# Kernel optimization log

Hardware: AMD Instinct MI355X
Metric: run time of the kernel (lower is better)

Reference implementation:

```python
import jax, jax.numpy as jnp
import numpy as np

# Model dims (match init_kwargs)
B, L, D = 1, 2048, 1024
DI = 2048          # D_inner
N = 16             # SSM state size
DR = 64            # delta_rank
K = 4              # conv_1d_size
EPS = 1e-5
DELTA_MIN, DELTA_MAX, DELTA_FLOOR = 1e-3, 1e-1, 1e-4


def setup_inputs() -> dict:
    key = jax.random.key(0)
    ks = jax.random.split(key, 9)
    g = lambda i, shape, scale: (jax.random.normal(ks[i], shape, jnp.float32) * scale)
    x = g(0, (B, L, D), 1.0)
    rms_w = jnp.ones((D,), jnp.float32)
    in_proj_w = g(1, (D, 2 * DI), D ** -0.5)           # Linear D -> 2*DI, no bias
    conv_w = g(2, (DI, K), 0.3)                         # depthwise conv kernel
    conv_b = g(3, (DI,), 0.1)
    bcd_w = g(4, (DI, 2 * N + DR), DI ** -0.5)          # to_BCdelta, no bias
    dup_w = g(5, (DR, DI), DR ** -0.5)                  # delta_upscale weight
    # delta_upscale bias: inverse-softplus of log-uniform samples in [delta_min, delta_max]
    u = jax.random.uniform(ks[6], (DI,), jnp.float32)
    samples = jnp.clip(jnp.exp(u * (np.log(DELTA_MAX) - np.log(DELTA_MIN)) + np.log(DELTA_MIN)), DELTA_FLOOR)
    dup_b = samples + jnp.log(-jnp.expm1(-samples))
    # log(-A) with A = -[1..N] repeated over channels (S4D-real init)
    log_minus_A = jnp.tile(jnp.log(jnp.arange(1, N + 1, dtype=jnp.float32))[None, :], (DI, 1))
    D_param = jnp.ones((DI,), jnp.float32)              # skip parameter D
    out_proj_w = g(7, (DI, D), DI ** -0.5)              # Linear DI -> D, no bias
    return {"x": x, "rms_w": rms_w, "in_proj_w": in_proj_w, "conv_w": conv_w,
            "conv_b": conv_b, "bcd_w": bcd_w, "dup_w": dup_w, "dup_b": dup_b,
            "log_minus_A": log_minus_A, "D_param": D_param, "out_proj_w": out_proj_w}


def reference(x, rms_w, in_proj_w, conv_w, conv_b, bcd_w, dup_w, dup_b,
              log_minus_A, D_param, out_proj_w):
    b, l, _ = x.shape
    # RMSNorm
    xn = x * jax.lax.rsqrt(jnp.mean(x * x, axis=-1, keepdims=True) + EPS) * rms_w
    # in_proj and split into ssm branch / gating residual branch
    proj = xn @ in_proj_w                                  # (b,l,2*DI)
    xs, res = proj[..., :DI], proj[..., DI:]
    # causal depthwise conv1d (torch pads K-1 both sides then truncates -> left-pad only)
    xp = jnp.pad(xs, ((0, 0), (K - 1, 0), (0, 0)))         # (b,l+K-1,DI)
    conv = sum(xp[:, k:k + l, :] * conv_w[:, k] for k in range(K)) + conv_b
    xc = jax.nn.silu(conv)                                 # (b,l,DI)
    # S6 block
    bcd = xc @ bcd_w                                       # (b,l,DR+2N)
    delta_lr = bcd[..., :DR]
    Bm = bcd[..., DR:DR + N]                               # (b,l,N)
    Cm = bcd[..., DR + N:]                                 # (b,l,N)
    delta = jax.nn.softplus(delta_lr @ dup_w + dup_b)      # (b,l,DI)
    A = -jnp.exp(log_minus_A)                              # (DI,N)
    A_bar = jnp.exp(jnp.einsum('bld,dn->bldn', delta, A))  # (b,l,DI,N)
    B_bar_x = jnp.einsum('bld,bln,bld->bldn', delta, Bm, xc)
    # sequential selective scan: h_t = A_bar_t * h_{t-1} + B_bar_x_t
    def step(h, ab_bx):
        ab, bx = ab_bx
        h = ab * h + bx
        return h, h
    h0 = jnp.zeros((b, DI, N), x.dtype)
    _, hs = jax.lax.scan(step, h0, (jnp.swapaxes(A_bar, 0, 1), jnp.swapaxes(B_bar_x, 0, 1)))
    # hs: (l,b,DI,N); project out with C and add skip D
    y = jnp.einsum('bln,lbdn->bld', Cm, hs) + xc * D_param
    # gate, out_proj, residual
    y = y * jax.nn.silu(res)
    return y @ out_proj_w + x
```

## Files before the change

### kernel.cpp

```cpp
#include <hip/hip_runtime.h>
#include <hip/hip_bf16.h>
#include <math.h>

#define Lseq 2048
#define Dmod 1024
#define DI   2048
#define Nst  16
#define DRr  64
#define NCHUNK 32
#define LCHUNK 64
#define SPLITK 16

typedef unsigned short u16;
typedef float  f32x4  __attribute__((ext_vector_type(4)));
typedef short  short8 __attribute__((ext_vector_type(8)));

__device__ __forceinline__ float sigmoidf_(float x) { return 1.f / (1.f + expf(-x)); }
__device__ __forceinline__ float softplusf_(float x) {
    return fmaxf(x, 0.f) + log1pf(expf(-fabsf(x)));
}
__device__ __forceinline__ u16 f2bf(float x) {
    union { float f; unsigned u; } v; v.f = x;
    unsigned r = (v.u + 0x7fffu + ((v.u >> 16) & 1u)) >> 16;
    return (u16)r;
}
__device__ __forceinline__ float bf2f(u16 h) {
    union { unsigned u; float f; } v; v.u = ((unsigned)h) << 16; return v.f;
}
__device__ __forceinline__ void async16(const void* g, void* l) {
    __builtin_amdgcn_global_load_lds((__attribute__((address_space(1))) void*)g,
                                     (__attribute__((address_space(3))) void*)l, 16, 0, 0);
}

struct __align__(8) u16x4 { u16 x, y, z, w; };

__global__ __launch_bounds__(256) void rmsnorm_split_k(const float* __restrict__ x,
                                                       const float* __restrict__ w,
                                                       u16* __restrict__ xh,
                                                       u16* __restrict__ xl) {
    int row = blockIdx.x;
    int tid = threadIdx.x;
    float4 v = reinterpret_cast<const float4*>(x + (size_t)row * Dmod)[tid];
    float ss = v.x * v.x + v.y * v.y + v.z * v.z + v.w * v.w;
    #pragma unroll
    for (int m = 32; m >= 1; m >>= 1) ss += __shfl_xor(ss, m);
    __shared__ float s4[4];
    if ((tid & 63) == 0) s4[tid >> 6] = ss;
    __syncthreads();
    float tot = s4[0] + s4[1] + s4[2] + s4[3];
    float scale = rsqrtf(tot * (1.0f / Dmod) + 1e-5f);
    float4 wv = reinterpret_cast<const float4*>(w)[tid];
    float o[4] = {v.x * scale * wv.x, v.y * scale * wv.y,
                  v.z * scale * wv.z, v.w * scale * wv.w};
    u16x4 H, L;
    u16* hp = &H.x; u16* lp = &L.x;
    #pragma unroll
    for (int q = 0; q < 4; q++) {
        u16 h = f2bf(o[q]); hp[q] = h; lp[q] = f2bf(o[q] - bf2f(h));
    }
    reinterpret_cast<u16x4*>(xh + (size_t)row * Dmod)[tid] = H;
    reinterpret_cast<u16x4*>(xl + (size_t)row * Dmod)[tid] = L;
}

__global__ __launch_bounds__(256) void wsplitT_k(const float* __restrict__ W, int R, int Cn,
                                                 u16* __restrict__ Th, u16* __restrict__ Tl) {
    __shared__ float t[32][33];
    int r0 = blockIdx.y * 32, c0 = blockIdx.x * 32;
    int tr = threadIdx.x >> 3;
    int tc4 = (threadIdx.x & 7) * 4;
    float4 v = *reinterpret_cast<const float4*>(&W[(size_t)(r0 + tr) * Cn + c0 + tc4]);
    t[tr][tc4 + 0] = v.x; t[tr][tc4 + 1] = v.y;
    t[tr][tc4 + 2] = v.z; t[tr][tc4 + 3] = v.w;
    __syncthreads();
    u16x4 H, L;
    u16* hp = &H.x; u16* lp = &L.x;
    #pragma unroll
    for (int q = 0; q < 4; q++) {
        float xv = t[tc4 + q][tr];
        u16 h = f2bf(xv); hp[q] = h; lp[q] = f2bf(xv - bf2f(h));
    }
    size_t o = (size_t)(c0 + tr) * R + r0 + tc4;
    *reinterpret_cast<u16x4*>(&Th[o]) = H;
    *reinterpret_cast<u16x4*>(&Tl[o]) = L;
}

template <int BM, int BN, int EPI>
__global__ __launch_bounds__(256) void gemm_mfma3(
    const u16* __restrict__ Ah, const u16* __restrict__ Al,
    const u16* __restrict__ Bh, const u16* __restrict__ Bl,
    float* __restrict__ C, float* __restrict__ C2, const float* __restrict__ aux,
    int M, int N, int K) {
    constexpr int BK = 32;
    constexpr int MF = BM / 32, NF = BN / 32;
    constexpr int CH_A = BM / 16, CH_B = BN / 16;
    __shared__ u16 AhT[BM][BK], AlT[BM][BK], BhT[BN][BK], BlT[BN][BK];
    const int tid = threadIdx.x, lane = tid & 63, wid = tid >> 6;
    const int wr = wid >> 1, wc = wid & 1;
    const int lr = lane & 15, lk = (lane >> 4) * 8;
    const int bm0 = blockIdx.y * BM, bn0 = blockIdx.x * BN;
    const int srow = lane >> 2, scol = (lane & 3) * 8;

    int kbeg = 0, kend = K;
    if (EPI == 5) {
        int ks = K / gridDim.z;
        kbeg = blockIdx.z * ks;
        kend = kbeg + ks;
    }

    f32x4 acc[MF][NF];
    #pragma unroll
    for (int i = 0; i < MF; i++)
        #pragma unroll
        for (int j = 0; j < NF; j++) acc[i][j] = (f32x4){0.f, 0.f, 0.f, 0.f};

    for (int k0 = kbeg; k0 < kend; k0 += BK) {
        int ci = 0;
        #pragma unroll
        for (int c = 0; c < CH_A; c++, ci++) if ((ci & 3) == wid) {
            size_t g = (size_t)(bm0 + c * 16 + srow) * K + (k0 + scol);
            async16(Ah + g, (u16*)&AhT[0][0] + c * 512 + lane * 8);
        }
        #pragma unroll
        for (int c = 0; c < CH_A; c++, ci++) if ((ci & 3) == wid) {
            size_t g = (size_t)(bm0 + c * 16 + srow) * K + (k0 + scol);
            async16(Al + g, (u16*)&AlT[0][0] + c * 512 + lane * 8);
        }
        #pragma unroll
        for (int c = 0; c < CH_B; c++, ci++) if ((ci & 3) == wid) {
            size_t g = (size_t)(bn0 + c * 16 + srow) * K + (k0 + scol);
            async16(Bh + g, (u16*)&BhT[0][0] + c * 512 + lane * 8);
        }
        #pragma unroll
        for (int c = 0; c < CH_B; c++, ci++) if ((ci & 3) == wid) {
            size_t g = (size_t)(bn0 + c * 16 + srow) * K + (k0 + scol);
            async16(Bl + g, (u16*)&BlT[0][0] + c * 512 + lane * 8);
        }
        __syncthreads();

        short8 ah[MF], al[MF], bh[NF], bl[NF];
        #pragma unroll
        for (int i = 0; i < MF; i++) {
            int r = wr * (MF * 16) + i * 16 + lr;
            ah[i] = *(const short8*)&AhT[r][lk];
            al[i] = *(const short8*)&AlT[r][lk];
        }
        #pragma unroll
        for (int j = 0; j < NF; j++) {
            int r = wc * (NF * 16) + j * 16 + lr;
            bh[j] = *(const short8*)&BhT[r][lk];
            bl[j] = *(const short8*)&BlT[r][lk];
        }
        #pragma unroll
        for (int i = 0; i < MF; i++)
            #pragma unroll
            for (int j = 0; j < NF; j++) {
                acc[i][j] = __builtin_amdgcn_mfma_f32_16x16x32_bf16(ah[i], bh[j], acc[i][j], 0, 0, 0);
                acc[i][j] = __builtin_amdgcn_mfma_f32_16x16x32_bf16(ah[i], bl[j], acc[i][j], 0, 0, 0);
                acc[i][j] = __builtin_amdgcn_mfma_f32_16x16x32_bf16(al[i], bh[j], acc[i][j], 0, 0, 0);
            }
        __syncthreads();
    }

    float* Cp = C;
    if (EPI == 5) Cp = C + (size_t)blockIdx.z * M * N;
    #pragma unroll
    for (int i = 0; i < MF; i++)
        #pragma unroll
        for (int j = 0; j < NF; j++) {
            int rowg = bm0 + wr * (MF * 16) + i * 16 + (lane >> 4) * 4;
            int colg = bn0 + wc * (NF * 16) + j * 16 + lr;
            #pragma unroll
            for (int q = 0; q < 4; q++) {
                float v = acc[i][j][q];
                if (EPI == 0 || EPI == 5) {
                    Cp[(size_t)(rowg + q) * N + colg] = v;
                } else if (EPI == 1) {
                    size_t idx = (size_t)(rowg + q) * N + colg;
                    C[idx] = v + aux[idx];
                } else if (EPI == 2) {
                    C[(size_t)(rowg + q) * N + colg] = softplusf_(v + aux[colg]);
                } else if (EPI == 4) {
                    if (colg < DI) C[(size_t)(rowg + q) * DI + colg] = v;
                    else C2[(size_t)(rowg + q) * DI + (colg - DI)] = v * sigmoidf_(v);
                }
            }
        }
}

__global__ __launch_bounds__(256) void bcd_reduce_k(const float* __restrict__ partial,
                                                    float* __restrict__ bcd,
                                                    u16* __restrict__ bH,
                                                    u16* __restrict__ bL) {
    const int NT = Lseq * 96;
    int t = blockIdx.x * 256 + threadIdx.x;
    float s = 0.f;
    #pragma unroll
    for (int z = 0; z < SPLITK; z++) s += partial[(size_t)z * NT + t];
    bcd[t] = s;
    int col = t % 96, row = t / 96;
    if (col < DRr) {
        u16 h = f2bf(s);
        bH[(size_t)row * DRr + col] = h;
        bL[(size_t)row * DRr + col] = f2bf(s - bf2f(h));
    }
}

__global__ __launch_bounds__(256) void conv_silu_k(const float* __restrict__ xs,
                                                   const float* __restrict__ cw,
                                                   const float* __restrict__ cb,
                                                   u16* __restrict__ xcH,
                                                   u16* __restrict__ xcL) {
    int d = blockIdx.x * 256 + threadIdx.x;
    int l = blockIdx.y;
    float4 w = reinterpret_cast<const float4*>(cw)[d];
    float wk[4] = {w.x, w.y, w.z, w.w};
    float s = cb[d];
    #pragma unroll
    for (int k = 0; k < 4; k++) {
        int ls = l - 3 + k;
        if (ls >= 0) s = fmaf(xs[(size_t)ls * DI + d], wk[k], s);
    }
    float v = s * sigmoidf_(s);
    size_t o = (size_t)l * DI + d;
    u16 h = f2bf(v);
    xcH[o] = h;
    xcL[o] = f2bf(v - bf2f(h));
}

__global__ __launch_bounds__(256) void scan1_k(const float* __restrict__ delta,
                                               const u16* __restrict__ xcH,
                                               const u16* __restrict__ xcL,
                                               const float* __restrict__ bcd,
                                               const float* __restrict__ lmA,
                                               float* __restrict__ Pb,
                                               float* __restrict__ Sb) {
    __shared__ float Bs[LCHUNK][16];
    const int tid = threadIdx.x;
    const int d = (blockIdx.x * 256 + tid) >> 1;
    const int half = tid & 1;
    const int c = blockIdx.y;
    const int l0 = c * LCHUNK;
    {
        int row = tid >> 2, q = (tid & 3) * 4;
        float4 v = *reinterpret_cast<const float4*>(&bcd[(size_t)(l0 + row) * 96 + DRr + q]);
        *reinterpret_cast<float4*>(&Bs[row][q]) = v;
    }
    __syncthreads();
    float negA[8], h[8];
    #pragma unroll
    for (int j = 0; j < 8; j++) {
        negA[j] = -__expf(lmA[(size_t)d * Nst + half * 8 + j]);
        h[j] = 0.f;
    }
    float sdv = 0.f;
    for (int l = 0; l < LCHUNK; ++l) {
        size_t o = (size_t)(l0 + l) * DI + d;
        float dv = delta[o];
        float xcv = bf2f(xcH[o]) + bf2f(xcL[o]);
        sdv += dv;
        float dvx = dv * xcv;
        #pragma unroll
        for (int j = 0; j < 8; j++) {
            float a = __expf(dv * negA[j]);
            h[j] = fmaf(a, h[j], dvx * Bs[l][half * 8 + j]);
        }
    }
    size_t base = ((size_t)c * DI + d) * Nst + half * 8;
    #pragma unroll
    for (int j = 0; j < 8; j++) {
        Pb[base + j] = __expf(sdv * negA[j]);
        Sb[base + j] = h[j];
    }
}

__global__ __launch_bounds__(256) void scan2_k(float* __restrict__ PH,
                                               const float* __restrict__ Sb) {
    int t = blockIdx.x * 256 + threadIdx.x;
    float H = 0.f;
    for (int c = 0; c < NCHUNK; c++) {
        size_t idx = (size_t)c * (DI * Nst) + t;
        float P = PH[idx], S = Sb[idx];
        PH[idx] = H;
        H = S + P * H;
    }
}

__global__ __launch_bounds__(256) void scan3_k(const float* __restrict__ delta,
                                               const u16* __restrict__ xcH,
                                               const u16* __restrict__ xcL,
                                               const float* __restrict__ bcd,
                                               const float* __restrict__ lmA,
                                               const float* __restrict__ Dp,
                                               const float* __restrict__ gate,
                                               const float* __restrict__ Hinit,
                                               u16* __restrict__ yH,
                                               u16* __restrict__ yL) {
    __shared__ float BCs[LCHUNK][32];
    const int tid = threadIdx.x;
    const int d = (blockIdx.x * 256 + tid) >> 1;
    const int half = tid & 1;
    const int c = blockIdx.y;
    const int l0 = c * LCHUNK;
    #pragma unroll
    for (int i = 0; i < 2; i++) {
        int idx = tid + 256 * i;
        int row = idx >> 3, q = (idx & 7) * 4;
        float4 v = *reinterpret_cast<const float4*>(&bcd[(size_t)(l0 + row) * 96 + DRr + q]);
        *reinterpret_cast<float4*>(&BCs[row][q]) = v;
    }
    __syncthreads();
    float negA[8], h[8];
    size_t hbase = ((size_t)c * DI + d) * Nst + half * 8;
    #pragma unroll
    for (int j = 0; j < 8; j++) {
        negA[j] = -__expf(lmA[(size_t)d * Nst + half * 8 + j]);
        h[j] = Hinit[hbase + j];
    }
    float Dpv = Dp[d];
    for (int l = 0; l < LCHUNK; ++l) {
        size_t o = (size_t)(l0 + l) * DI + d;
        float dv = delta[o];
        float xcv = bf2f(xcH[o]) + bf2f(xcL[o]);
        float dvx = dv * xcv;
        float yp = 0.f;
        #pragma unroll
        for (int j = 0; j < 8; j++) {
            float a = __expf(dv * negA[j]);
            h[j] = fmaf(a, h[j], dvx * BCs[l][half * 8 + j]);
            yp = fmaf(BCs[l][16 + half * 8 + j], h[j], yp);
        }
        yp += __shfl_xor(yp, 1);
        if (half == 0) {
            float yv = (yp + xcv * Dpv) * gate[o];
            u16 hq = f2bf(yv);
            yH[o] = hq;
            yL[o] = f2bf(yv - bf2f(hq));
        }
    }
}

extern "C" void kernel_launch(void* const* d_in, const int* in_sizes, int n_in,
                              void* d_out, int out_size, void* d_ws, size_t ws_size,
                              hipStream_t stream) {
    const float* x          = (const float*)d_in[0];
    const float* rms_w      = (const float*)d_in[1];
    const float* in_proj_w  = (const float*)d_in[2];
    const float* conv_w     = (const float*)d_in[3];
    const float* conv_b     = (const float*)d_in[4];
    const float* bcd_w      = (const float*)d_in[5];
    const float* dup_w      = (const float*)d_in[6];
    const float* dup_b      = (const float*)d_in[7];
    const float* lmA        = (const float*)d_in[8];
    const float* Dp         = (const float*)d_in[9];
    const float* out_proj_w = (const float*)d_in[10];
    float* out = (float*)d_out;
    char*  W   = (char*)d_ws;

    const size_t MB = 1ull << 20;
    u16*   WiH  = (u16*)(W + 0);
    u16*   WiL  = (u16*)(W + 8 * MB);
    float* delta= (float*)(W + 0);
    float* xs   = (float*)(W + 16 * MB);
    float* part = (float*)(W + 16 * MB);
    u16*   bwTH = (u16*)(W + 28 * MB);
    u16*   bwTL = (u16*)(W + 28 * MB + 384 * 1024);
    u16*   dwTH = (u16*)(W + 28 * MB + 768 * 1024);
    u16*   dwTL = (u16*)(W + 28 * MB + 1024 * 1024);
    u16*   bcdH = (u16*)(W + 28 * MB + 1280 * 1024);
    u16*   bcdL = (u16*)(W + 28 * MB + 1536 * 1024);
    float* Sb   = (float*)(W + 16 * MB);
    u16*   yH   = (u16*)(W + 16 * MB);
    u16*   yL   = (u16*)(W + 24 * MB);
    float* gate = (float*)(W + 32 * MB);
    u16*   xcH  = (u16*)(W + 48 * MB);
    u16*   xcL  = (u16*)(W + 56 * MB);
    u16*   xnH  = (u16*)(W + 64 * MB);
    u16*   xnL  = (u16*)(W + 68 * MB);
    u16*   WoH  = (u16*)(W + 64 * MB);
    u16*   WoL  = (u16*)(W + 68 * MB);
    float* bcd  = (float*)(W + 72 * MB);
    float* Pb   = (float*)(W + 73 * MB);

    rmsnorm_split_k<<<Lseq, 256, 0, stream>>>(x, rms_w, xnH, xnL);
    wsplitT_k<<<dim3(4096 / 32, 1024 / 32), 256, 0, stream>>>(in_proj_w, 1024, 4096, WiH, WiL);
    gemm_mfma3<128, 128, 4><<<dim3(4096 / 128, Lseq / 128), 256, 0, stream>>>(
        xnH, xnL, WiH, WiL, xs, gate, nullptr, Lseq, 2 * DI, Dmod);
    conv_silu_k<<<dim3(DI / 256, Lseq), 256, 0, stream>>>(xs, conv_w, conv_b, xcH, xcL);
    wsplitT_k<<<dim3(1024 / 32, 2048 / 32), 256, 0, stream>>>(out_proj_w, 2048, 1024, WoH, WoL);
    wsplitT_k<<<dim3(96 / 32, 2048 / 32), 256, 0, stream>>>(bcd_w, 2048, 96, bwTH, bwTL);
    wsplitT_k<<<dim3(2048 / 32, 64 / 32), 256, 0, stream>>>(dup_w, 64, 2048, dwTH, dwTL);
    gemm_mfma3<128, 96, 5><<<dim3(1, Lseq / 128, SPLITK), 256, 0, stream>>>(
        xcH, xcL, bwTH, bwTL, part, nullptr, nullptr, Lseq, 96, DI);
    bcd_reduce_k<<<Lseq * 96 / 256, 256, 0, stream>>>(part, bcd, bcdH, bcdL);
    gemm_mfma3<128, 128, 2><<<dim3(DI / 128, Lseq / 128), 256, 0, stream>>>(
        bcdH, bcdL, dwTH, dwTL, delta, nullptr, dup_b, Lseq, DI, DRr);
    scan1_k<<<dim3(16, NCHUNK), 256, 0, stream>>>(delta, xcH, xcL, bcd, lmA, Pb, Sb);
    scan2_k<<<dim3(DI * Nst / 256), 256, 0, stream>>>(Pb, Sb);
    scan3_k<<<dim3(16, NCHUNK), 256, 0, stream>>>(delta, xcH, xcL, bcd, lmA, Dp, gate, Pb, yH, yL);
    gemm_mfma3<64, 128, 1><<<dim3(Dmod / 128, Lseq / 64), 256, 0, stream>>>(
        yH, yL, WoH, WoL, out, nullptr, x, Lseq, Dmod, DI);
}
```

Measured before the change: 292.1 us.

## Split-K out_proj with residual reduce, merge weight-split launches, retile in_proj

The out_proj GEMM becomes a 2-way split-K into partial buffers, and a new reduce kernel sums the partials and adds the residual x. The three small weight split/transpose kernels are merged into one launch. The in_proj GEMM switches to 128x64 tiles, which gives more blocks for better CU occupancy. The trade-off is extra partial-sum memory traffic and one more kernel launch, in exchange for more parallelism across the device.

```diff
diff --git a/kernel.cpp b/kernel.cpp
--- a/kernel.cpp
+++ b/kernel.cpp
@@ -62,10 +62,10 @@
     reinterpret_cast<u16x4*>(xl + (size_t)row * Dmod)[tid] = L;
 }
 
-__global__ __launch_bounds__(256) void wsplitT_k(const float* __restrict__ W, int R, int Cn,
-                                                 u16* __restrict__ Th, u16* __restrict__ Tl) {
-    __shared__ float t[32][33];
-    int r0 = blockIdx.y * 32, c0 = blockIdx.x * 32;
+__device__ __forceinline__ void wsplit_body(const float* __restrict__ W, int R, int Cn,
+                                            int bx, int by, float (*t)[33],
+                                            u16* __restrict__ Th, u16* __restrict__ Tl) {
+    int r0 = by * 32, c0 = bx * 32;
     int tr = threadIdx.x >> 3;
     int tc4 = (threadIdx.x & 7) * 4;
     float4 v = *reinterpret_cast<const float4*>(&W[(size_t)(r0 + tr) * Cn + c0 + tc4]);
@@ -82,6 +82,31 @@
     size_t o = (size_t)(c0 + tr) * R + r0 + tc4;
     *reinterpret_cast<u16x4*>(&Th[o]) = H;
     *reinterpret_cast<u16x4*>(&Tl[o]) = L;
+}
+
+__global__ __launch_bounds__(256) void wsplitT_k(const float* __restrict__ W, int R, int Cn,
+                                                 u16* __restrict__ Th, u16* __restrict__ Tl) {
+    __shared__ float t[32][33];
+    wsplit_body(W, R, Cn, blockIdx.x, blockIdx.y, t, Th, Tl);
+}
+
+__global__ __launch_bounds__(256) void wsplit3_k(const float* __restrict__ Wo,
+                                                 const float* __restrict__ Wb,
+                                                 const float* __restrict__ Wd,
+                                                 u16* WoH, u16* WoL,
+                                                 u16* bwTH, u16* bwTL,
+                                                 u16* dwTH, u16* dwTL) {
+    __shared__ float t[32][33];
+    int b = blockIdx.x;
+    if (b < 2048) {
+        wsplit_body(Wo, 2048, 1024, b & 31, b >> 5, t, WoH, WoL);
+    } else if (b < 2240) {
+        int bb = b - 2048;
+        wsplit_body(Wb, 2048, 96, bb % 3, bb / 3, t, bwTH, bwTL);
+    } else {
+        int bb = b - 2240;
+        wsplit_body(Wd, 64, 2048, bb & 63, bb >> 6, t, dwTH, dwTL);
+    }
 }
 
 template <int BM, int BN, int EPI>
@@ -172,11 +197,8 @@
             #pragma unroll
             for (int q = 0; q < 4; q++) {
                 float v = acc[i][j][q];
-                if (EPI == 0 || EPI == 5) {
+                if (EPI == 5) {
                     Cp[(size_t)(rowg + q) * N + colg] = v;
-                } else if (EPI == 1) {
-                    size_t idx = (size_t)(rowg + q) * N + colg;
-                    C[idx] = v + aux[idx];
                 } else if (EPI == 2) {
                     C[(size_t)(rowg + q) * N + colg] = softplusf_(v + aux[colg]);
                 } else if (EPI == 4) {
@@ -203,6 +225,20 @@
         bH[(size_t)row * DRr + col] = h;
         bL[(size_t)row * DRr + col] = f2bf(s - bf2f(h));
     }
+}
+
+__global__ __launch_bounds__(256) void out_reduce_k(const float* __restrict__ part,
+                                                    const float* __restrict__ x,
+                                                    float* __restrict__ out) {
+    int t = blockIdx.x * 256 + threadIdx.x;
+    const size_t NT = (size_t)Lseq * Dmod;
+    float4 a = reinterpret_cast<const float4*>(part)[t];
+    float4 b = reinterpret_cast<const float4*>(part + NT)[t];
+    float4 xv = reinterpret_cast<const float4*>(x)[t];
+    float4 o;
+    o.x = a.x + b.x + xv.x; o.y = a.y + b.y + xv.y;
+    o.z = a.z + b.z + xv.z; o.w = a.w + b.w + xv.w;
+    reinterpret_cast<float4*>(out)[t] = o;
 }
 
 __global__ __launch_bounds__(256) void conv_silu_k(const float* __restrict__ xs,
@@ -360,6 +396,7 @@
     u16*   WiH  = (u16*)(W + 0);
     u16*   WiL  = (u16*)(W + 8 * MB);
     float* delta= (float*)(W + 0);
+    float* opart= (float*)(W + 0);
     float* xs   = (float*)(W + 16 * MB);
     float* part = (float*)(W + 16 * MB);
     u16*   bwTH = (u16*)(W + 28 * MB);
@@ -383,12 +420,11 @@
 
     rmsnorm_split_k<<<Lseq, 256, 0, stream>>>(x, rms_w, xnH, xnL);
     wsplitT_k<<<dim3(4096 / 32, 1024 / 32), 256, 0, stream>>>(in_proj_w, 1024, 4096, WiH, WiL);
-    gemm_mfma3<128, 128, 4><<<dim3(4096 / 128, Lseq / 128), 256, 0, stream>>>(
+    gemm_mfma3<128, 64, 4><<<dim3(4096 / 64, Lseq / 128), 256, 0, stream>>>(
         xnH, xnL, WiH, WiL, xs, gate, nullptr, Lseq, 2 * DI, Dmod);
     conv_silu_k<<<dim3(DI / 256, Lseq), 256, 0, stream>>>(xs, conv_w, conv_b, xcH, xcL);
-    wsplitT_k<<<dim3(1024 / 32, 2048 / 32), 256, 0, stream>>>(out_proj_w, 2048, 1024, WoH, WoL);
-    wsplitT_k<<<dim3(96 / 32, 2048 / 32), 256, 0, stream>>>(bcd_w, 2048, 96, bwTH, bwTL);
-    wsplitT_k<<<dim3(2048 / 32, 64 / 32), 256, 0, stream>>>(dup_w, 64, 2048, dwTH, dwTL);
+    wsplit3_k<<<2368, 256, 0, stream>>>(out_proj_w, bcd_w, dup_w,
+                                        WoH, WoL, bwTH, bwTL, dwTH, dwTL);
     gemm_mfma3<128, 96, 5><<<dim3(1, Lseq / 128, SPLITK), 256, 0, stream>>>(
         xcH, xcL, bwTH, bwTL, part, nullptr, nullptr, Lseq, 96, DI);
     bcd_reduce_k<<<Lseq * 96 / 256, 256, 0, stream>>>(part, bcd, bcdH, bcdL);
@@ -397,6 +433,7 @@
     scan1_k<<<dim3(16, NCHUNK), 256, 0, stream>>>(delta, xcH, xcL, bcd, lmA, Pb, Sb);
     scan2_k<<<dim3(DI * Nst / 256), 256, 0, stream>>>(Pb, Sb);
     scan3_k<<<dim3(16, NCHUNK), 256, 0, stream>>>(delta, xcH, xcL, bcd, lmA, Dp, gate, Pb, yH, yL);
-    gemm_mfma3<64, 128, 1><<<dim3(Dmod / 128, Lseq / 64), 256, 0, stream>>>(
-        yH, yL, WoH, WoL, out, nullptr, x, Lseq, Dmod, DI);
-}
+    gemm_mfma3<128, 64, 5><<<dim3(Dmod / 64, Lseq / 128, 2), 256, 0, stream>>>(
+        yH, yL, WoH, WoL, opart, nullptr, nullptr, Lseq, Dmod, DI);
+    out_reduce_k<<<Lseq * Dmod / 1024, 256, 0, stream>>>(opart, x, out);
+}
```

Result: faster. 281.4 us (-3.7%).
